# Kernel tuning notes

Hardware: AMD Instinct MI355X
Metric: run time of the kernel (lower is better)

Reference implementation:

```python
import jax, jax.numpy as jnp
import numpy as np

N_NODES = 100000
N_EDGES = 1600000
D = 128
L = 3
D_OUT = 64


def setup_inputs() -> dict:
    key = jax.random.key(0)
    ks = jax.random.split(key, 6)
    x = jax.random.normal(ks[0], (N_NODES, D), dtype=jnp.float32)
    edge_index = jax.random.randint(ks[1], (2, N_EDGES), 0, N_NODES, dtype=jnp.int64)
    # Kaiming-ish init scale for linear layers
    s = 1.0 / np.sqrt(D)
    W_rel = jax.random.normal(ks[2], (L, D, D), dtype=jnp.float32) * s
    b_rel = jnp.zeros((L, D), dtype=jnp.float32)
    W_root = jax.random.normal(ks[3], (L, D, D), dtype=jnp.float32) * s
    fc_w = jax.random.normal(ks[4], (D_OUT, D), dtype=jnp.float32) * s
    fc_b = jnp.zeros((D_OUT,), dtype=jnp.float32)
    return {"x": x, "edge_index": edge_index, "W_rel": W_rel, "b_rel": b_rel,
            "W_root": W_root, "fc_w": fc_w, "fc_b": fc_b}


def reference(x, edge_index, W_rel, b_rel, W_root, fc_w, fc_b):
    # PyG GraphConv (aggr='add'): x_i' = W_root x_i + W_rel * sum_{j in N(i)} x_j + b
    src, dst = edge_index[0], edge_index[1]
    n = x.shape[0]
    num_layers = W_rel.shape[0]  # static small loop over layers
    for l in range(num_layers):
        agg = jax.ops.segment_sum(x[src], dst, num_segments=n)  # [N, D] scatter-add of gathered neighbor feats
        x = agg @ W_rel[l].T + b_rel[l] + x @ W_root[l].T
    return x @ fc_w.T + fc_b
```

## Files before the change

### kernel.cpp

```cpp
#include <hip/hip_runtime.h>


typedef short bf16x8 __attribute__((ext_vector_type(8)));
typedef float f32x4 __attribute__((ext_vector_type(4)));

#define CAPB 8192

__device__ inline float bf2f(unsigned short u) {
    union { unsigned int i; float f; } v; v.i = ((unsigned int)u) << 16; return v.f;
}
__device__ inline unsigned short f2bf(float f) {
    union { float f; unsigned int i; } v; v.f = f;
    unsigned int r = v.i + 0x7FFFu + ((v.i >> 16) & 1u);
    return (unsigned short)(r >> 16);
}

__global__ __launch_bounds__(512) void prep_kernel(
    const float* __restrict__ Wr2, const float* __restrict__ Wo2,
    const float* __restrict__ fcw, float* __restrict__ K0_2, float* __restrict__ K1_2,
    const int* __restrict__ src, const int* __restrict__ dst,
    int* __restrict__ gcur, unsigned int* __restrict__ bucketed, int e, int NA, int NB) {
    int b = blockIdx.x, t = threadIdx.x;
    if (b < 64) {
        if (t < 256) {
            int matid = b >> 5;
            const float* W = matid ? Wr2 : Wo2;
            float* K = matid ? K1_2 : K0_2;
            int i = t & 127;
            int j = (b & 31) * 2 + (t >> 7);
            float acc = 0.f;
            for (int k = 0; k < 128; k++) acc += W[k * 128 + i] * fcw[j * 128 + k];
            K[i * 64 + j] = acc;
        }
        return;
    }
    b -= 64;
    if (b < NA) {
        __shared__ int sHist[512], sScan[512], sExcl[512], sGbase[512];
        __shared__ unsigned int lbuf[2048];
        __shared__ unsigned short lbkt[2048];
        int e0 = b * 2048;
        int cnt = e - e0; if (cnt > 2048) cnt = 2048;
        sHist[t] = 0;
        __syncthreads();
        unsigned int pk[4]; int bk[4];
#pragma unroll
        for (int k = 0; k < 4; k++) {
            int j = t + k * 512;
            if (j < cnt) {
                int d = dst[e0 + j], s = src[e0 + j];
                bk[k] = d >> 8;
                pk[k] = ((unsigned int)s << 8) | (unsigned int)(d & 255);
                atomicAdd(&sHist[bk[k]], 1);
            } else bk[k] = -1;
        }
        __syncthreads();
        int h = sHist[t];
        if (t < NB && h > 0) sGbase[t] = atomicAdd(&gcur[t], h);
        else sGbase[t] = 0;
        int xv = h; sScan[t] = xv; __syncthreads();
        for (int o = 1; o < 512; o <<= 1) {
            int y = (t >= o) ? sScan[t - o] : 0;
            __syncthreads();
            xv += y; sScan[t] = xv;
            __syncthreads();
        }
        sExcl[t] = xv - h;
        sHist[t] = 0;
        __syncthreads();
#pragma unroll
        for (int k = 0; k < 4; k++) {
            if (bk[k] >= 0) {
                int r = atomicAdd(&sHist[bk[k]], 1);
                int pos = sExcl[bk[k]] + r;
                lbuf[pos] = pk[k];
                lbkt[pos] = (unsigned short)bk[k];
            }
        }
        __syncthreads();
        for (int j = t; j < cnt; j += 512) {
            int b2 = lbkt[j];
            int idx = sGbase[b2] + (j - sExcl[b2]);
            if (idx < CAPB) bucketed[(size_t)b2 * CAPB + idx] = lbuf[j];
        }
    }
}

__global__ __launch_bounds__(256) void partB_kernel(
    const unsigned int* __restrict__ bucketed, const int* __restrict__ gcur,
    int* __restrict__ deg, int* __restrict__ start, int* __restrict__ csr, int n) {
    int b = blockIdx.x, t = threadIdx.x;
    __shared__ int ldeg[256], lscan[256], red[256];
    __shared__ int csr_base_s;
    int cnt = gcur[b]; if (cnt > CAPB) cnt = CAPB;
    int part = 0;
    for (int q = t; q < b; q += 256) { int c = gcur[q]; part += (c > CAPB ? CAPB : c); }
    red[t] = part; __syncthreads();
    for (int o = 128; o > 0; o >>= 1) { if (t < o) red[t] += red[t + o]; __syncthreads(); }
    if (t == 0) csr_base_s = red[0];
    ldeg[t] = 0;
    __syncthreads();
    const unsigned int* bd = bucketed + (size_t)b * CAPB;
    for (int j = t; j < cnt; j += 256) atomicAdd(&ldeg[bd[j] & 255], 1);
    __syncthreads();
    int h = ldeg[t];
    int xv = h; lscan[t] = xv; __syncthreads();
    for (int o = 1; o < 256; o <<= 1) {
        int y = (t >= o) ? lscan[t - o] : 0;
        __syncthreads();
        xv += y; lscan[t] = xv;
        __syncthreads();
    }
    int excl = xv - h;
    int csr_base = csr_base_s;
    int node = b * 256 + t;
    if (node < n) { deg[node] = h; start[node] = csr_base + excl; }
    __syncthreads();
    lscan[t] = excl;
    ldeg[t] = 0;
    __syncthreads();
    for (int j = t; j < cnt; j += 256) {
        unsigned int pkd = bd[j];
        int d = pkd & 255;
        int r = atomicAdd(&ldeg[d], 1);
        csr[csr_base + lscan[d] + r] = (int)(pkd >> 8);
    }
}

__global__ __launch_bounds__(256) void stage2_kernel(
    const float* __restrict__ Wr1, const float* __restrict__ Wo1,
    const float* __restrict__ K0_2, const float* __restrict__ K1_2,
    float* __restrict__ K0_1, float* __restrict__ K1_1, float* __restrict__ K2_1) {
    int b = blockIdx.x, t = threadIdx.x;
    int matid = b >> 5;
    int i = t & 127;
    int j = (b & 31) * 2 + (t >> 7);
    float acc = 0.f;
    if (matid == 0) {
        for (int k = 0; k < 128; k++) acc += Wo1[k * 128 + i] * K0_2[k * 64 + j];
        K0_1[i * 64 + j] = acc;
    } else if (matid == 1) {
        for (int k = 0; k < 128; k++)
            acc += Wr1[k * 128 + i] * K0_2[k * 64 + j] + Wo1[k * 128 + i] * K1_2[k * 64 + j];
        K1_1[i * 64 + j] = acc;
    } else {
        for (int k = 0; k < 128; k++) acc += Wr1[k * 128 + i] * K1_2[k * 64 + j];
        K2_1[i * 64 + j] = acc;
    }
}

__global__ __launch_bounds__(256) void stage3_kernel(
    const float* __restrict__ Wr0, const float* __restrict__ Wo0,
    const float* __restrict__ K0_1, const float* __restrict__ K1_1, const float* __restrict__ K2_1,
    const float* __restrict__ K0_2, const float* __restrict__ K1_2,
    const float* __restrict__ br, const float* __restrict__ fcw, const float* __restrict__ fcb,
    unsigned short* __restrict__ Nw, float* __restrict__ Bv) {
    int b = blockIdx.x, t = threadIdx.x;
    if (b < 128) {
        int matid = b >> 5;
        int i = t & 127;
        int o = (b & 31) * 2 + (t >> 7);
        float acc = 0.f;
        if (matid == 0) {
            for (int k = 0; k < 128; k++) acc += Wo0[k * 128 + i] * K0_1[k * 64 + o];
        } else if (matid == 1) {
            for (int k = 0; k < 128; k++)
                acc += Wr0[k * 128 + i] * K0_1[k * 64 + o] + Wo0[k * 128 + i] * K1_1[k * 64 + o];
        } else if (matid == 2) {
            for (int k = 0; k < 128; k++)
                acc += Wr0[k * 128 + i] * K1_1[k * 64 + o] + Wo0[k * 128 + i] * K2_1[k * 64 + o];
        } else {
            for (int k = 0; k < 128; k++) acc += Wr0[k * 128 + i] * K2_1[k * 64 + o];
        }
        int p = ((o & 3) << 4) | (o >> 2);
        Nw[p * 512 + matid * 128 + i] = f2bf(acc);
        return;
    }
    const float* br0 = br;
    const float* br1 = br + 128;
    const float* br2 = br + 256;
    int j = t & 63;
    int which = t >> 6;
    if (which == 0) {
        float acc = fcb[j];
        for (int k = 0; k < 128; k++) acc += br2[k] * fcw[j * 128 + k];
        for (int k = 0; k < 128; k++) acc += br1[k] * K0_2[k * 64 + j];
        for (int k = 0; k < 128; k++) acc += br0[k] * K0_1[k * 64 + j];
        Bv[j] = acc;
    } else if (which == 1) {
        float acc = 0.f;
        for (int k = 0; k < 128; k++) acc += br1[k] * K1_2[k * 64 + j];
        for (int k = 0; k < 128; k++) acc += br0[k] * K1_1[k * 64 + j];
        Bv[64 + j] = acc;
    } else if (which == 2) {
        float acc = 0.f;
        for (int k = 0; k < 128; k++) acc += br0[k] * K2_1[k * 64 + j];
        Bv[128 + j] = acc;
    }
}

__global__ __launch_bounds__(256, 4) void gemm_u_kernel(
    const float* __restrict__ x, const unsigned short* __restrict__ Nw,
    unsigned short* __restrict__ U, int n, int NGB) {
    __shared__ unsigned short Blds[8192];
    int bid   = blockIdx.x;
    int matid = (bid >> 3) & 3;
    int blk   = (bid >> 5) * 8 + (bid & 7);
    if (blk >= NGB) return;
    int tid   = threadIdx.x;

    {
        const uint4* nw4 = (const uint4*)Nw;
        uint4* lds4 = (uint4*)Blds;
        for (int g = tid; g < 1024; g += 256) {
            int slot = g & 63;
            int kq   = g >> 6;
            lds4[g] = nw4[(size_t)slot * 64 + matid * 16 + kq];
        }
    }
    __syncthreads();

    int wave = tid >> 6;
    int lane = tid & 63;
    int m    = lane & 15;
    int quad = lane >> 4;
    size_t n64 = (size_t)n * 64;
    unsigned short* up = U + (size_t)matid * n64;

    const int t0 = blk * 16 + wave * 4;

    float4 v[8];
    {
        int arow = t0 * 16 + m; if (arow >= n) arow = n - 1;
        const float* xr = x + (size_t)arow * 128 + quad * 8;
#pragma unroll
        for (int kk = 0; kk < 4; kk++) {
            v[2 * kk]     = *(const float4*)(xr + kk * 32);
            v[2 * kk + 1] = *(const float4*)(xr + kk * 32 + 4);
        }
    }

#pragma unroll
    for (int it = 0; it < 4; it++) {
        int row0 = (t0 + it) * 16;
        if (row0 >= n) break;

        bf16x8 a[4];
#pragma unroll
        for (int kk = 0; kk < 4; kk++) {
            float4 v0 = v[2 * kk], v1 = v[2 * kk + 1];
            a[kk][0] = (short)f2bf(v0.x); a[kk][1] = (short)f2bf(v0.y);
            a[kk][2] = (short)f2bf(v0.z); a[kk][3] = (short)f2bf(v0.w);
            a[kk][4] = (short)f2bf(v1.x); a[kk][5] = (short)f2bf(v1.y);
            a[kk][6] = (short)f2bf(v1.z); a[kk][7] = (short)f2bf(v1.w);
        }

        if (it < 3) {
            int arow = row0 + 16 + m; if (arow >= n) arow = n - 1;
            const float* xr = x + (size_t)arow * 128 + quad * 8;
#pragma unroll
            for (int kk = 0; kk < 4; kk++) {
                v[2 * kk]     = *(const float4*)(xr + kk * 32);
                v[2 * kk + 1] = *(const float4*)(xr + kk * 32 + 4);
            }
        }

        f32x4 acc[4];
#pragma unroll
        for (int t = 0; t < 4; t++) acc[t] = (f32x4){0.f, 0.f, 0.f, 0.f};
#pragma unroll
        for (int kk = 0; kk < 4; kk++) {
            bf16x8 bq[4];
#pragma unroll
            for (int t = 0; t < 4; t++)
                bq[t] = *(const bf16x8*)(Blds + ((kk * 4 + quad) * 64 + t * 16 + m) * 8);
#pragma unroll
            for (int t = 0; t < 4; t++)
                acc[t] = __builtin_amdgcn_mfma_f32_16x16x32_bf16(a[kk], bq[t], acc[t], 0, 0, 0);
        }

#pragma unroll
        for (int r = 0; r < 4; r++) {
            int orow = row0 + quad * 4 + r;
            if (orow < n) {
                ushort4 o4;
                o4.x = f2bf(acc[0][r]); o4.y = f2bf(acc[1][r]);
                o4.z = f2bf(acc[2][r]); o4.w = f2bf(acc[3][r]);
                *(ushort4*)(up + (size_t)orow * 64 + m * 4) = o4;
            }
        }
    }
}

template <int MODE>
__global__ __launch_bounds__(256) void agg64_kernel(
    const unsigned short* __restrict__ in, const unsigned short* __restrict__ addv,
    const int* __restrict__ csr, const int* __restrict__ start, const int* __restrict__ deg,
    unsigned short* __restrict__ outb, float* __restrict__ outf,
    const float* __restrict__ Bv, int* __restrict__ d2w, const int* __restrict__ d2r, int n) {
    int tid = threadIdx.x;
    int fl  = tid & 7;
    int node = blockIdx.x * 32 + (tid >> 3);
    if (node >= n) return;

    float b0[8], b1[8], b2[8];
    if (MODE == 2) {
#pragma unroll
        for (int j = 0; j < 8; j++) {
            int o = fl * 8 + j;
            b0[j] = Bv[o]; b1[j] = Bv[64 + o]; b2[j] = Bv[128 + o];
        }
    }

    int s0 = start[node];
    int d  = deg[node];

    float acc[8];
#pragma unroll
    for (int j = 0; j < 8; j++) acc[j] = 0.f;
    int dsum = 0;

    int d8 = d & ~7;
    for (int e0 = 0; e0 < d8; e0 += 8) {
        int sv[8];
#pragma unroll
        for (int k = 0; k < 8; k++) sv[k] = csr[s0 + e0 + k];
#pragma unroll
        for (int k = 0; k < 8; k++) {
            bf16x8 v = *(const bf16x8*)(in + (size_t)sv[k] * 64 + fl * 8);
#pragma unroll
            for (int j = 0; j < 8; j++) acc[j] += bf2f((unsigned short)v[j]);
            if (MODE == 0 && fl == 0) dsum += deg[sv[k]];
        }
    }
    for (int i = d8; i < d; i++) {
        int s = csr[s0 + i];
        bf16x8 v = *(const bf16x8*)(in + (size_t)s * 64 + fl * 8);
#pragma unroll
        for (int j = 0; j < 8; j++) acc[j] += bf2f((unsigned short)v[j]);
        if (MODE == 0 && fl == 0) dsum += deg[s];
    }
    if (MODE == 0 && fl == 0) d2w[node] = dsum;

    bf16x8 av = *(const bf16x8*)(addv + (size_t)node * 64 + fl * 8);
    if (MODE < 2) {
        bf16x8 o;
#pragma unroll
        for (int j = 0; j < 8; j++) o[j] = (short)f2bf(acc[j] + bf2f((unsigned short)av[j]));
        *(bf16x8*)(outb + (size_t)node * 64 + fl * 8) = o;
    } else {
        float dg = (float)d;
        float dd = (float)d2r[node];
        float ov[8];
#pragma unroll
        for (int j = 0; j < 8; j++)
            ov[j] = acc[j] + bf2f((unsigned short)av[j]) + b0[j] + dg * b1[j] + dd * b2[j];
        float* op = outf + (size_t)node * 64 + fl * 8;
        *(float4*)(op)     = make_float4(ov[0], ov[1], ov[2], ov[3]);
        *(float4*)(op + 4) = make_float4(ov[4], ov[5], ov[6], ov[7]);
    }
}

extern "C" void kernel_launch(void* const* d_in, const int* in_sizes, int n_in,
                              void* d_out, int out_size, void* d_ws, size_t ws_size,
                              hipStream_t stream) {
    const float* x      = (const float*)d_in[0];
    const int*   ei     = (const int*)d_in[1];
    const float* W_rel  = (const float*)d_in[2];
    const float* b_rel  = (const float*)d_in[3];
    const float* W_root = (const float*)d_in[4];
    const float* fc_w   = (const float*)d_in[5];
    const float* fc_b   = (const float*)d_in[6];

    const int n = in_sizes[0] / 128;
    const int e = in_sizes[1] / 2;
    const int* src = ei;
    const int* dst = ei + e;

    const int NB  = (n + 255) >> 8;
    const int NA  = (e + 2047) / 2048;
    const int NT  = (n + 15) / 16;
    const int NGB = (NT + 15) / 16;
    const int NGBp = (NGB + 7) & ~7;

    char* p = (char*)d_ws;
    auto take = [&](size_t bytes) -> void* {
        void* r = (void*)p;
        p += (bytes + 255) & ~(size_t)255;
        return r;
    };
    unsigned short* U  = (unsigned short*)take((size_t)n * 256 * 2);
    unsigned short* w1 = (unsigned short*)take((size_t)n * 64 * 2);
    unsigned short* w2 = (unsigned short*)take((size_t)n * 64 * 2);
    int* deg    = (int*)take((size_t)n * 4);
    int* start  = (int*)take((size_t)n * 4);
    int* d2     = (int*)take((size_t)n * 4);
    int* csr    = (int*)take((size_t)e * 4);
    unsigned int* bucketed = (unsigned int*)take((size_t)NB * CAPB * 4);
    int* gcur   = (int*)take((size_t)NB * 4);
    float* K0_2 = (float*)take(128 * 64 * 4);
    float* K1_2 = (float*)take(128 * 64 * 4);
    float* K0_1 = (float*)take(128 * 64 * 4);
    float* K1_1 = (float*)take(128 * 64 * 4);
    float* K2_1 = (float*)take(128 * 64 * 4);
    unsigned short* Nw = (unsigned short*)take(64 * 512 * 2);
    float* Bv   = (float*)take(192 * 4);

    size_t n64 = (size_t)n * 64;
    unsigned short* u0 = U;
    unsigned short* u1 = U + n64;
    unsigned short* u2 = U + 2 * n64;
    unsigned short* u3 = U + 3 * n64;

    hipMemsetAsync(gcur, 0, (size_t)NB * 4, stream);
    prep_kernel<<<64 + NA, 512, 0, stream>>>(
        W_rel + 2 * 16384, W_root + 2 * 16384, fc_w, K0_2, K1_2,
        src, dst, gcur, bucketed, e, NA, NB);
    partB_kernel<<<NB, 256, 0, stream>>>(bucketed, gcur, deg, start, csr, n);
    stage2_kernel<<<96, 256, 0, stream>>>(
        W_rel + 16384, W_root + 16384, K0_2, K1_2, K0_1, K1_1, K2_1);
    stage3_kernel<<<129, 256, 0, stream>>>(
        W_rel, W_root, K0_1, K1_1, K2_1, K0_2, K1_2, b_rel, fc_w, fc_b, Nw, Bv);

    gemm_u_kernel<<<NGBp * 4, 256, 0, stream>>>(x, Nw, U, n, NGB);

    const int AGB = (n + 31) / 32;
    agg64_kernel<0><<<AGB, 256, 0, stream>>>(
        u3, u2, csr, start, deg, w1, nullptr, nullptr, d2, nullptr, n);
    agg64_kernel<1><<<AGB, 256, 0, stream>>>(
        w1, u1, csr, start, deg, w2, nullptr, nullptr, nullptr, nullptr, n);
    agg64_kernel<2><<<AGB, 256, 0, stream>>>(
        w2, u0, csr, start, deg, nullptr, (float*)d_out, Bv, nullptr, d2, n);
}
```

Baseline: 315.6 us.

## Fuse weight-chain precompute stages into one kernel and drop memset

Merges the three weight-folding stages (fc_w through layer 2, 1, 0 plus bias folding) into a single 64-block kernel where each block owns one output column and keeps intermediate vectors in shared memory. The same kernel zeroes the bucket cursors, so the separate memset and two kernel launches go away, and prep_kernel no longer carries the weight blocks. The cost is that the serial weight chain now runs on only 64 blocks ahead of the edge bucketing instead of alongside it, which lengthens that part of the critical path.

```diff
diff --git a/kernel.cpp b/kernel.cpp
--- a/kernel.cpp
+++ b/kernel.cpp
@@ -15,26 +15,94 @@
     return (unsigned short)(r >> 16);
 }
 
+__global__ __launch_bounds__(256) void stages_kernel(
+    const float* __restrict__ Wr0, const float* __restrict__ Wo0,
+    const float* __restrict__ Wr1, const float* __restrict__ Wo1,
+    const float* __restrict__ Wr2, const float* __restrict__ Wo2,
+    const float* __restrict__ fcw, const float* __restrict__ fcb,
+    const float* __restrict__ br, unsigned short* __restrict__ Nw,
+    float* __restrict__ Bv, int* __restrict__ gcur, int NB) {
+    int o = blockIdx.x;
+    int t = threadIdx.x;
+    __shared__ float c02[128], c12[128], c01[128], c11[128], c21[128];
+    __shared__ float redbuf[3][128];
+
+    if (o == 0) {
+        for (int q = t; q < NB; q += 256) gcur[q] = 0;
+    }
+
+    const float* fo = fcw + (size_t)o * 128;
+    int i  = t & 127;
+    int hi = t >> 7;
+
+    {
+        const float* W = hi ? Wr2 : Wo2;
+        float acc = 0.f;
+        for (int k = 0; k < 128; k++) acc += W[k * 128 + i] * fo[k];
+        (hi ? c12 : c02)[i] = acc;
+    }
+    __syncthreads();
+
+    if (!hi) {
+        float a0 = 0.f, a2 = 0.f;
+        for (int k = 0; k < 128; k++) {
+            float w1o = Wo1[k * 128 + i], w1r = Wr1[k * 128 + i];
+            a0 += w1o * c02[k];
+            a2 += w1r * c12[k];
+        }
+        c01[i] = a0; c21[i] = a2;
+    } else {
+        float a1 = 0.f;
+        for (int k = 0; k < 128; k++)
+            a1 += Wr1[k * 128 + i] * c02[k] + Wo1[k * 128 + i] * c12[k];
+        c11[i] = a1;
+    }
+    __syncthreads();
+
+    {
+        int p = ((o & 3) << 4) | (o >> 2);
+        if (!hi) {
+            float a0 = 0.f, a2 = 0.f;
+            for (int k = 0; k < 128; k++) {
+                float w0 = Wo0[k * 128 + i], wr = Wr0[k * 128 + i];
+                a0 += w0 * c01[k];
+                a2 += wr * c11[k] + w0 * c21[k];
+            }
+            Nw[(size_t)p * 512 + 0 * 128 + i] = f2bf(a0);
+            Nw[(size_t)p * 512 + 2 * 128 + i] = f2bf(a2);
+        } else {
+            float a1 = 0.f, a3 = 0.f;
+            for (int k = 0; k < 128; k++) {
+                float w0 = Wo0[k * 128 + i], wr = Wr0[k * 128 + i];
+                a1 += wr * c01[k] + w0 * c11[k];
+                a3 += wr * c21[k];
+            }
+            Nw[(size_t)p * 512 + 1 * 128 + i] = f2bf(a1);
+            Nw[(size_t)p * 512 + 3 * 128 + i] = f2bf(a3);
+        }
+    }
+
+    const float* br0 = br;
+    const float* br1 = br + 128;
+    const float* br2 = br + 256;
+    if (!hi) {
+        redbuf[0][i] = br2[i] * fo[i] + br1[i] * c02[i] + br0[i] * c01[i];
+        redbuf[1][i] = br1[i] * c12[i] + br0[i] * c11[i];
+        redbuf[2][i] = br0[i] * c21[i];
+    }
+    __syncthreads();
+    int w = t >> 6, lane = t & 63;
+    if (w < 3) {
+        float v = redbuf[w][lane] + redbuf[w][lane + 64];
+        for (int off = 32; off; off >>= 1) v += __shfl_down(v, off);
+        if (lane == 0) Bv[w * 64 + o] = v + (w == 0 ? fcb[o] : 0.f);
+    }
+}
+
 __global__ __launch_bounds__(512) void prep_kernel(
-    const float* __restrict__ Wr2, const float* __restrict__ Wo2,
-    const float* __restrict__ fcw, float* __restrict__ K0_2, float* __restrict__ K1_2,
     const int* __restrict__ src, const int* __restrict__ dst,
     int* __restrict__ gcur, unsigned int* __restrict__ bucketed, int e, int NA, int NB) {
     int b = blockIdx.x, t = threadIdx.x;
-    if (b < 64) {
-        if (t < 256) {
-            int matid = b >> 5;
-            const float* W = matid ? Wr2 : Wo2;
-            float* K = matid ? K1_2 : K0_2;
-            int i = t & 127;
-            int j = (b & 31) * 2 + (t >> 7);
-            float acc = 0.f;
-            for (int k = 0; k < 128; k++) acc += W[k * 128 + i] * fcw[j * 128 + k];
-            K[i * 64 + j] = acc;
-        }
-        return;
-    }
-    b -= 64;
     if (b < NA) {
         __shared__ int sHist[512], sScan[512], sExcl[512], sGbase[512];
         __shared__ unsigned int lbuf[2048];
@@ -124,78 +192,6 @@
         int d = pkd & 255;
         int r = atomicAdd(&ldeg[d], 1);
         csr[csr_base + lscan[d] + r] = (int)(pkd >> 8);
-    }
-}
-
-__global__ __launch_bounds__(256) void stage2_kernel(
-    const float* __restrict__ Wr1, const float* __restrict__ Wo1,
-    const float* __restrict__ K0_2, const float* __restrict__ K1_2,
-    float* __restrict__ K0_1, float* __restrict__ K1_1, float* __restrict__ K2_1) {
-    int b = blockIdx.x, t = threadIdx.x;
-    int matid = b >> 5;
-    int i = t & 127;
-    int j = (b & 31) * 2 + (t >> 7);
-    float acc = 0.f;
-    if (matid == 0) {
-        for (int k = 0; k < 128; k++) acc += Wo1[k * 128 + i] * K0_2[k * 64 + j];
-        K0_1[i * 64 + j] = acc;
-    } else if (matid == 1) {
-        for (int k = 0; k < 128; k++)
-            acc += Wr1[k * 128 + i] * K0_2[k * 64 + j] + Wo1[k * 128 + i] * K1_2[k * 64 + j];
-        K1_1[i * 64 + j] = acc;
-    } else {
-        for (int k = 0; k < 128; k++) acc += Wr1[k * 128 + i] * K1_2[k * 64 + j];
-        K2_1[i * 64 + j] = acc;
-    }
-}
-
-__global__ __launch_bounds__(256) void stage3_kernel(
-    const float* __restrict__ Wr0, const float* __restrict__ Wo0,
-    const float* __restrict__ K0_1, const float* __restrict__ K1_1, const float* __restrict__ K2_1,
-    const float* __restrict__ K0_2, const float* __restrict__ K1_2,
-    const float* __restrict__ br, const float* __restrict__ fcw, const float* __restrict__ fcb,
-    unsigned short* __restrict__ Nw, float* __restrict__ Bv) {
-    int b = blockIdx.x, t = threadIdx.x;
-    if (b < 128) {
-        int matid = b >> 5;
-        int i = t & 127;
-        int o = (b & 31) * 2 + (t >> 7);
-        float acc = 0.f;
-        if (matid == 0) {
-            for (int k = 0; k < 128; k++) acc += Wo0[k * 128 + i] * K0_1[k * 64 + o];
-        } else if (matid == 1) {
-            for (int k = 0; k < 128; k++)
-                acc += Wr0[k * 128 + i] * K0_1[k * 64 + o] + Wo0[k * 128 + i] * K1_1[k * 64 + o];
-        } else if (matid == 2) {
-            for (int k = 0; k < 128; k++)
-                acc += Wr0[k * 128 + i] * K1_1[k * 64 + o] + Wo0[k * 128 + i] * K2_1[k * 64 + o];
-        } else {
-            for (int k = 0; k < 128; k++) acc += Wr0[k * 128 + i] * K2_1[k * 64 + o];
-        }
-        int p = ((o & 3) << 4) | (o >> 2);
-        Nw[p * 512 + matid * 128 + i] = f2bf(acc);
-        return;
-    }
-    const float* br0 = br;
-    const float* br1 = br + 128;
-    const float* br2 = br + 256;
-    int j = t & 63;
-    int which = t >> 6;
-    if (which == 0) {
-        float acc = fcb[j];
-        for (int k = 0; k < 128; k++) acc += br2[k] * fcw[j * 128 + k];
-        for (int k = 0; k < 128; k++) acc += br1[k] * K0_2[k * 64 + j];
-        for (int k = 0; k < 128; k++) acc += br0[k] * K0_1[k * 64 + j];
-        Bv[j] = acc;
-    } else if (which == 1) {
-        float acc = 0.f;
-        for (int k = 0; k < 128; k++) acc += br1[k] * K1_2[k * 64 + j];
-        for (int k = 0; k < 128; k++) acc += br0[k] * K1_1[k * 64 + j];
-        Bv[64 + j] = acc;
-    } else if (which == 2) {
-        float acc = 0.f;
-        for (int k = 0; k < 128; k++) acc += br0[k] * K2_1[k * 64 + j];
-        Bv[128 + j] = acc;
     }
 }
 
@@ -398,11 +394,6 @@
     int* csr    = (int*)take((size_t)e * 4);
     unsigned int* bucketed = (unsigned int*)take((size_t)NB * CAPB * 4);
     int* gcur   = (int*)take((size_t)NB * 4);
-    float* K0_2 = (float*)take(128 * 64 * 4);
-    float* K1_2 = (float*)take(128 * 64 * 4);
-    float* K0_1 = (float*)take(128 * 64 * 4);
-    float* K1_1 = (float*)take(128 * 64 * 4);
-    float* K2_1 = (float*)take(128 * 64 * 4);
     unsigned short* Nw = (unsigned short*)take(64 * 512 * 2);
     float* Bv   = (float*)take(192 * 4);
 
@@ -412,15 +403,12 @@
     unsigned short* u2 = U + 2 * n64;
     unsigned short* u3 = U + 3 * n64;
 
-    hipMemsetAsync(gcur, 0, (size_t)NB * 4, stream);
-    prep_kernel<<<64 + NA, 512, 0, stream>>>(
-        W_rel + 2 * 16384, W_root + 2 * 16384, fc_w, K0_2, K1_2,
-        src, dst, gcur, bucketed, e, NA, NB);
+    stages_kernel<<<64, 256, 0, stream>>>(
+        W_rel, W_root, W_rel + 16384, W_root + 16384,
+        W_rel + 2 * 16384, W_root + 2 * 16384,
+        fc_w, fc_b, b_rel, Nw, Bv, gcur, NB);
+    prep_kernel<<<NA, 512, 0, stream>>>(src, dst, gcur, bucketed, e, NA, NB);
     partB_kernel<<<NB, 256, 0, stream>>>(bucketed, gcur, deg, start, csr, n);
-    stage2_kernel<<<96, 256, 0, stream>>>(
-        W_rel + 16384, W_root + 16384, K0_2, K1_2, K0_1, K1_1, K2_1);
-    stage3_kernel<<<129, 256, 0, stream>>>(
-        W_rel, W_root, K0_1, K1_1, K2_1, K0_2, K1_2, b_rel, fc_w, fc_b, Nw, Bv);
 
     gemm_u_kernel<<<NGBp * 4, 256, 0, stream>>>(x, Nw, U, n, NGB);
 
```

After: 307.6 us. 2.5% less time.
